# Kernel optimization log

Measured on AMD Instinct MI355X. Metric: run time of the kernel, lower is better.

The kernel has to match this reference:

```python
import jax, jax.numpy as jnp
import numpy as np

NB_FEATURES = 256
DIM_HEADS = 64
KERNEL_EPS = 1e-4


def _gaussian_orthogonal_random_matrix(nb_rows, nb_cols, seed=0):
    # Mirrors gaussian_orthogonal_random_matrix with scaling=0, qr_uniform_q=False.
    rng = np.random.default_rng(seed)
    blocks = []
    for _ in range(nb_rows // nb_cols):
        a = rng.standard_normal((nb_cols, nb_cols))
        qm, _ = np.linalg.qr(a)
        blocks.append(qm.T)
    rem = nb_rows - (nb_rows // nb_cols) * nb_cols
    if rem > 0:
        a = rng.standard_normal((nb_cols, nb_cols))
        qm, _ = np.linalg.qr(a)
        blocks.append(qm.T[:rem])
    final = np.concatenate(blocks, axis=0)
    multiplier = np.linalg.norm(rng.standard_normal((nb_rows, nb_cols)), axis=1)
    return (multiplier[:, None] * final).astype(np.float32)


def setup_inputs() -> dict:
    key = jax.random.key(0)
    kq, kk, kv = jax.random.split(key, 3)
    shape = (2, 16, 4096, DIM_HEADS)  # [b, h, n, dim_heads]
    q = jax.random.normal(kq, shape, dtype=jnp.float32)
    k = jax.random.normal(kk, shape, dtype=jnp.float32)
    v = jax.random.normal(kv, shape, dtype=jnp.float32)
    projection = jnp.asarray(_gaussian_orthogonal_random_matrix(NB_FEATURES, DIM_HEADS))
    return {"q": q, "k": k, "v": v, "projection": projection}


def _softmax_kernel(x, projection, is_query):
    # x: [b,h,n,d]; projection: [j,d]
    d = x.shape[-1]
    data_normalizer = d ** -0.25
    ratio = projection.shape[0] ** -0.5
    data_dash = jnp.einsum('bhnd,jd->bhnj', data_normalizer * x, projection)
    diag = jnp.sum(x * x, axis=-1, keepdims=True) * (0.5 * data_normalizer ** 2)  # [b,h,n,1]
    if is_query:
        m = jnp.max(data_dash, axis=-1, keepdims=True)
    else:
        m = jnp.max(data_dash)
    return ratio * (jnp.exp(data_dash - diag - m) + KERNEL_EPS)


def reference(q, k, v, projection):
    qp = _softmax_kernel(q, projection, is_query=True)   # [b,h,n,j]
    kp = _softmax_kernel(k, projection, is_query=False)  # [b,h,n,j]
    k_sum = jnp.sum(kp, axis=-2)                          # [b,h,j]
    d_inv = 1.0 / jnp.einsum('bhnj,bhj->bhn', qp, k_sum)  # [b,h,n]
    context = jnp.einsum('bhnj,bhne->bhje', kp, v)        # [b,h,j,e]
    out = jnp.einsum('bhje,bhnj,bhn->bhne', context, qp, d_inv)
    return out
```

## Files before the change

### kernel.cpp

```cpp
#include <hip/hip_runtime.h>

#define NFEAT 256
#define DHEAD 64
#define NSEQ  4096
#define NHEADS 32

constexpr float NORM_C  = 0.35355339059327373f;
constexpr float RATIO_C = 0.0625f;
constexpr float DIAG_C  = 0.0625f;
constexpr float KEPS_C  = 1e-4f;

using v8s = __attribute__((ext_vector_type(8))) short;
using v4f = __attribute__((ext_vector_type(4))) float;
union Frag8 { v8s v; ushort u[8]; };

__device__ __forceinline__ ushort bf16h(float x) {
  unsigned u = __float_as_uint(x);
  return (ushort)((u + 0x7FFFu + ((u >> 16) & 1)) >> 16);
}
__device__ __forceinline__ float bf16f(ushort h) {
  return __uint_as_float(((unsigned)h) << 16);
}
__device__ __forceinline__ unsigned enc_f(float f) {
  unsigned u = __float_as_uint(f);
  return (u & 0x80000000u) ? ~u : (u | 0x80000000u);
}
__device__ __forceinline__ float dec_f(unsigned e) {
  return (e & 0x80000000u) ? __uint_as_float(e ^ 0x80000000u) : __uint_as_float(~e);
}

#define MFMA(a, b, c) __builtin_amdgcn_mfma_f32_16x16x32_bf16((a), (b), (c), 0, 0, 0)

__global__ void prep_kernel(const float* __restrict__ proj,
                            ushort* __restrict__ P2hi, ushort* __restrict__ P2lo) {
  int i = blockIdx.x * 256 + threadIdx.x;
  if (i < NFEAT * DHEAD) {
    int j = i >> 6, d = i & 63;
    float x = NORM_C * proj[i];
    ushort h = bf16h(x);
    int off = ((d >> 3) * NFEAT + j) * 8 + (d & 7);
    P2hi[off] = h;
    P2lo[off] = bf16h(x - bf16f(h));
  }
}

__global__ __launch_bounds__(256, 2) void kmax_kernel(
    const float* __restrict__ kk, const ushort* __restrict__ P2hi,
    const ushort* __restrict__ P2lo, unsigned* __restrict__ kmax_u) {
  __shared__ __align__(16) ushort PhiL[NFEAT * DHEAD];
  __shared__ __align__(16) ushort PloL[NFEAT * DHEAD];
  __shared__ float wred[4];
  const int t = threadIdx.x, lane = t & 63, w = t >> 6;
  const int cl = lane & 15, q = lane >> 4;
  const int mw = w & 1, jw = w >> 1;
  const int head = blockIdx.x >> 4, slab = blockIdx.x & 15;
  for (int i = t; i < 4096; i += 256) {
    ((float4*)PhiL)[i] = ((const float4*)P2hi)[i];
    ((float4*)PloL)[i] = ((const float4*)P2lo)[i];
  }
  const float* abase =
      kk + ((size_t)(head * NSEQ + slab * 256 + mw * 16 + cl)) * DHEAD + q * 8;
  float4 pa0 = *(const float4*)(abase);
  float4 pa1 = *(const float4*)(abase + 4);
  float4 pa2 = *(const float4*)(abase + 32);
  float4 pa3 = *(const float4*)(abase + 36);
  __syncthreads();
  float mx = -3.0e38f;
  for (int c = 0; c < 8; ++c) {
    float af[2][8] = {{pa0.x, pa0.y, pa0.z, pa0.w, pa1.x, pa1.y, pa1.z, pa1.w},
                      {pa2.x, pa2.y, pa2.z, pa2.w, pa3.x, pa3.y, pa3.z, pa3.w}};
    Frag8 ah[2], al[2];
#pragma unroll
    for (int ks = 0; ks < 2; ++ks)
#pragma unroll
      for (int i = 0; i < 8; ++i) {
        ushort h = bf16h(af[ks][i]);
        ah[ks].u[i] = h;
        al[ks].u[i] = bf16h(af[ks][i] - bf16f(h));
      }
    if (c < 7) {
      const float* nx = abase + (size_t)(c + 1) * 32 * DHEAD;
      pa0 = *(const float4*)(nx);
      pa1 = *(const float4*)(nx + 4);
      pa2 = *(const float4*)(nx + 32);
      pa3 = *(const float4*)(nx + 36);
    }
    v4f acc[8];
#pragma unroll
    for (int jt = 0; jt < 8; ++jt) acc[jt] = (v4f){0.f, 0.f, 0.f, 0.f};
#pragma unroll
    for (int ks = 0; ks < 2; ++ks)
#pragma unroll
      for (int jt = 0; jt < 8; ++jt) {
        int pidx = ((ks * 4 + q) * NFEAT + jw * 128 + jt * 16 + cl) * 8;
        v8s bh = *(const v8s*)&PhiL[pidx];
        v8s bl = *(const v8s*)&PloL[pidx];
        acc[jt] = MFMA(ah[ks].v, bh, acc[jt]);
        acc[jt] = MFMA(ah[ks].v, bl, acc[jt]);
        acc[jt] = MFMA(al[ks].v, bh, acc[jt]);
      }
#pragma unroll
    for (int jt = 0; jt < 8; ++jt)
#pragma unroll
      for (int r = 0; r < 4; ++r) mx = fmaxf(mx, acc[jt][r]);
  }
  for (int s = 1; s < 64; s <<= 1) mx = fmaxf(mx, __shfl_xor(mx, s));
  if (lane == 0) wred[w] = mx;
  __syncthreads();
  if (t == 0)
    atomicMax(kmax_u,
              enc_f(fmaxf(fmaxf(wred[0], wred[1]), fmaxf(wred[2], wred[3]))));
}

#define KPS 40
#define VTS 40
__global__ __launch_bounds__(512, 2) void kctx_kernel(
    const float* __restrict__ kk, const float* __restrict__ vv,
    const ushort* __restrict__ P2hi, const ushort* __restrict__ P2lo,
    const unsigned* __restrict__ kmax_u, float* __restrict__ ksum,
    float* __restrict__ ctx) {
  __shared__ __align__(16) ushort PhiL[NFEAT * DHEAD];
  __shared__ __align__(16) ushort PloL[NFEAT * DHEAD];
  __shared__ __align__(16) ushort kphi[NFEAT * KPS];
  __shared__ __align__(16) ushort kplo[NFEAT * KPS];
  __shared__ __align__(16) ushort vthi[DHEAD * VTS];
  __shared__ __align__(16) ushort vtlo[DHEAD * VTS];
  __shared__ float diag[32];
  const int t = threadIdx.x, lane = t & 63, w = t >> 6;
  const int cl = lane & 15, q = lane >> 4;
  const int mw = w & 1, jq = w >> 1;
  const int head = blockIdx.x >> 3, slab = blockIdx.x & 7;
  const float m = dec_f(*kmax_u);
  for (int i = t; i < 4096; i += 512) {
    ((float4*)PhiL)[i] = ((const float4*)P2hi)[i];
    ((float4*)PloL)[i] = ((const float4*)P2lo)[i];
  }
  float ksacc[4] = {0.f, 0.f, 0.f, 0.f};
  v4f ctxacc[4][2];
#pragma unroll
  for (int jj = 0; jj < 4; ++jj)
#pragma unroll
    for (int et = 0; et < 2; ++et) ctxacc[jj][et] = (v4f){0.f, 0.f, 0.f, 0.f};

  const float* abase =
      kk + ((size_t)(head * NSEQ + slab * 512 + mw * 16 + cl)) * DHEAD + q * 8;
  const int vrow = t >> 4, ve0 = (t & 15) * 4;
  const float* vbase =
      vv + ((size_t)(head * NSEQ + slab * 512 + vrow)) * DHEAD + ve0;
  float4 pa0 = *(const float4*)(abase);
  float4 pa1 = *(const float4*)(abase + 4);
  float4 pa2 = *(const float4*)(abase + 32);
  float4 pa3 = *(const float4*)(abase + 36);
  float4 pv0 = *(const float4*)(vbase);

  for (int c = 0; c < 16; ++c) {
    __syncthreads();
    {
      float fv[4] = {pv0.x, pv0.y, pv0.z, pv0.w};
#pragma unroll
      for (int cc = 0; cc < 4; ++cc) {
        int e = ve0 + cc;
        ushort h = bf16h(fv[cc]);
        vthi[e * VTS + vrow] = h;
        vtlo[e * VTS + vrow] = bf16h(fv[cc] - bf16f(h));
      }
    }
    float af[2][8] = {{pa0.x, pa0.y, pa0.z, pa0.w, pa1.x, pa1.y, pa1.z, pa1.w},
                      {pa2.x, pa2.y, pa2.z, pa2.w, pa3.x, pa3.y, pa3.z, pa3.w}};
    Frag8 ah[2], al[2];
    float ssq = 0.f;
#pragma unroll
    for (int ks = 0; ks < 2; ++ks)
#pragma unroll
      for (int i = 0; i < 8; ++i) {
        float x = af[ks][i];
        ssq = fmaf(x, x, ssq);
        ushort h = bf16h(x);
        ah[ks].u[i] = h;
        al[ks].u[i] = bf16h(x - bf16f(h));
      }
    if (c < 15) {
      const float* nx = abase + (size_t)(c + 1) * 32 * DHEAD;
      pa0 = *(const float4*)(nx);
      pa1 = *(const float4*)(nx + 4);
      pa2 = *(const float4*)(nx + 32);
      pa3 = *(const float4*)(nx + 36);
      pv0 = *(const float4*)(vbase + (size_t)(c + 1) * 32 * DHEAD);
    }
    v4f acc[4];
#pragma unroll
    for (int jt = 0; jt < 4; ++jt) acc[jt] = (v4f){0.f, 0.f, 0.f, 0.f};
#pragma unroll
    for (int ks = 0; ks < 2; ++ks)
#pragma unroll
      for (int jt = 0; jt < 4; ++jt) {
        int pidx = ((ks * 4 + q) * NFEAT + jq * 64 + jt * 16 + cl) * 8;
        v8s bh = *(const v8s*)&PhiL[pidx];
        v8s bl = *(const v8s*)&PloL[pidx];
        acc[jt] = MFMA(ah[ks].v, bh, acc[jt]);
        acc[jt] = MFMA(ah[ks].v, bl, acc[jt]);
        acc[jt] = MFMA(al[ks].v, bh, acc[jt]);
      }
    {
      float s2 = ssq;
      s2 += __shfl_xor(s2, 16);
      s2 += __shfl_xor(s2, 32);
      if (jq == 0 && q == 0) diag[mw * 16 + cl] = DIAG_C * s2;
    }
    __syncthreads();
#pragma unroll
    for (int jt = 0; jt < 4; ++jt) {
      int j = jq * 64 + jt * 16 + cl;
      float kv[4];
#pragma unroll
      for (int r = 0; r < 4; ++r) {
        int row = mw * 16 + q * 4 + r;
        float e_ = RATIO_C * (__expf(acc[jt][r] - diag[row] - m) + KEPS_C);
        kv[r] = e_;
        ksacc[jt] += e_;
      }
#pragma unroll
      for (int p = 0; p < 2; ++p) {
        ushort h0 = bf16h(kv[2 * p]), h1 = bf16h(kv[2 * p + 1]);
        ushort l0 = bf16h(kv[2 * p] - bf16f(h0));
        ushort l1 = bf16h(kv[2 * p + 1] - bf16f(h1));
        int ui = j * KPS + mw * 16 + q * 4 + 2 * p;
        *(uint*)&kphi[ui] = (uint)h0 | ((uint)h1 << 16);
        *(uint*)&kplo[ui] = (uint)l0 | ((uint)l1 << 16);
      }
    }
    __syncthreads();
    const int eh = w & 1, jq3 = w >> 1;
    v8s bhv[2], blv[2];
#pragma unroll
    for (int et = 0; et < 2; ++et) {
      int e = (eh * 2 + et) * 16 + cl;
      bhv[et] = *(const v8s*)&vthi[e * VTS + q * 8];
      blv[et] = *(const v8s*)&vtlo[e * VTS + q * 8];
    }
#pragma unroll
    for (int jj = 0; jj < 4; ++jj) {
      int jrow = jq3 * 64 + jj * 16 + cl;
      v8s ah2 = *(const v8s*)&kphi[jrow * KPS + q * 8];
      v8s al2 = *(const v8s*)&kplo[jrow * KPS + q * 8];
#pragma unroll
      for (int et = 0; et < 2; ++et) {
        ctxacc[jj][et] = MFMA(ah2, bhv[et], ctxacc[jj][et]);
        ctxacc[jj][et] = MFMA(ah2, blv[et], ctxacc[jj][et]);
        ctxacc[jj][et] = MFMA(al2, bhv[et], ctxacc[jj][et]);
      }
    }
  }
#pragma unroll
  for (int jt = 0; jt < 4; ++jt) {
    float s = ksacc[jt];
    s += __shfl_xor(s, 16);
    s += __shfl_xor(s, 32);
    if (q == 0) atomicAdd(&ksum[head * NFEAT + jq * 64 + jt * 16 + cl], s);
  }
  {
    const int eh = w & 1, jq3 = w >> 1;
#pragma unroll
    for (int jj = 0; jj < 4; ++jj)
#pragma unroll
      for (int et = 0; et < 2; ++et)
#pragma unroll
        for (int r = 0; r < 4; ++r) {
          int j = jq3 * 64 + jj * 16 + q * 4 + r;
          int e = (eh * 2 + et) * 16 + cl;
          atomicAdd(&ctx[((size_t)head * NFEAT + j) * DHEAD + e],
                    ctxacc[jj][et][r]);
        }
  }
}

__global__ void ctxprep_kernel(const float* __restrict__ ctx,
                               ushort* __restrict__ ctxThi,
                               ushort* __restrict__ ctxTlo) {
  __shared__ float tile[64 * 65];
  const int head = blockIdx.x >> 2, jb = blockIdx.x & 3, t = threadIdx.x;
#pragma unroll
  for (int i = 0; i < 16; ++i) {
    int idx = t + i * 256;
    int jj = idx >> 6, e = idx & 63;
    tile[jj * 65 + e] = ctx[((size_t)head * NFEAT + jb * 64 + jj) * DHEAD + e];
  }
  __syncthreads();
#pragma unroll
  for (int i = 0; i < 16; ++i) {
    int idx = t + i * 256;
    int e = idx >> 6, jj = idx & 63;
    float x = tile[jj * 65 + e];
    ushort h = bf16h(x);
    size_t o = ((size_t)head * DHEAD + e) * NFEAT + jb * 64 + jj;
    ctxThi[o] = h;
    ctxTlo[o] = bf16h(x - bf16f(h));
  }
}

#define QPS 264
#define OS 68
__global__ __launch_bounds__(512, 2) void qout_kernel(
    const float* __restrict__ qq, const ushort* __restrict__ P2hi,
    const ushort* __restrict__ P2lo, const float* __restrict__ ksum,
    const ushort* __restrict__ ctxThi, const ushort* __restrict__ ctxTlo,
    float* __restrict__ out) {
  __shared__ __align__(16) ushort PhiL[NFEAT * DHEAD];
  __shared__ __align__(16) ushort PloL[NFEAT * DHEAD];
  __shared__ __align__(16) ushort qphi[32 * QPS];
  __shared__ __align__(16) ushort qplo[32 * QPS];
  __shared__ __align__(16) float souts[32 * OS];
  __shared__ float diag[32];
  __shared__ float mpart[4][32], dpart[4][32];
  const int t = threadIdx.x, lane = t & 63, w = t >> 6;
  const int cl = lane & 15, q = lane >> 4;
  const int mw = w & 1, jq = w >> 1;
  const int mw3 = w & 1, et3 = w >> 1;
  const int head = blockIdx.x >> 3, slab = blockIdx.x & 7;
  for (int i = t; i < 4096; i += 512) {
    ((float4*)PhiL)[i] = ((const float4*)P2hi)[i];
    ((float4*)PloL)[i] = ((const float4*)P2lo)[i];
  }
  float ksl[4];
#pragma unroll
  for (int jt = 0; jt < 4; ++jt)
    ksl[jt] = ksum[head * NFEAT + jq * 64 + jt * 16 + cl];
  v8s bhr[8], blr[8];
  {
    const size_t bo = ((size_t)head * DHEAD + et3 * 16 + cl) * NFEAT + q * 8;
#pragma unroll
    for (int ks8 = 0; ks8 < 8; ++ks8) {
      bhr[ks8] = *(const v8s*)(ctxThi + bo + ks8 * 32);
      blr[ks8] = *(const v8s*)(ctxTlo + bo + ks8 * 32);
    }
  }
  const float* abase =
      qq + ((size_t)(head * NSEQ + slab * 512 + mw * 16 + cl)) * DHEAD + q * 8;
  float4 pa0 = *(const float4*)(abase);
  float4 pa1 = *(const float4*)(abase + 4);
  float4 pa2 = *(const float4*)(abase + 32);
  float4 pa3 = *(const float4*)(abase + 36);
  __syncthreads();

  for (int c = 0; c < 16; ++c) {
    const int row0 = slab * 512 + c * 32;
    float af[2][8] = {{pa0.x, pa0.y, pa0.z, pa0.w, pa1.x, pa1.y, pa1.z, pa1.w},
                      {pa2.x, pa2.y, pa2.z, pa2.w, pa3.x, pa3.y, pa3.z, pa3.w}};
    Frag8 ah[2], al[2];
    float ssq = 0.f;
#pragma unroll
    for (int ks = 0; ks < 2; ++ks)
#pragma unroll
      for (int i = 0; i < 8; ++i) {
        float x = af[ks][i];
        ssq = fmaf(x, x, ssq);
        ushort h = bf16h(x);
        ah[ks].u[i] = h;
        al[ks].u[i] = bf16h(x - bf16f(h));
      }
    if (c < 15) {
      const float* nx = abase + (size_t)(c + 1) * 32 * DHEAD;
      pa0 = *(const float4*)(nx);
      pa1 = *(const float4*)(nx + 4);
      pa2 = *(const float4*)(nx + 32);
      pa3 = *(const float4*)(nx + 36);
    }
    v4f acc[4];
#pragma unroll
    for (int jt = 0; jt < 4; ++jt) acc[jt] = (v4f){0.f, 0.f, 0.f, 0.f};
#pragma unroll
    for (int ks = 0; ks < 2; ++ks)
#pragma unroll
      for (int jt = 0; jt < 4; ++jt) {
        int pidx = ((ks * 4 + q) * NFEAT + jq * 64 + jt * 16 + cl) * 8;
        v8s bh = *(const v8s*)&PhiL[pidx];
        v8s bl = *(const v8s*)&PloL[pidx];
        acc[jt] = MFMA(ah[ks].v, bh, acc[jt]);
        acc[jt] = MFMA(ah[ks].v, bl, acc[jt]);
        acc[jt] = MFMA(al[ks].v, bh, acc[jt]);
      }
    {
      float s2 = ssq;
      s2 += __shfl_xor(s2, 16);
      s2 += __shfl_xor(s2, 32);
      if (jq == 0 && q == 0) diag[mw * 16 + cl] = DIAG_C * s2;
    }
#pragma unroll
    for (int r = 0; r < 4; ++r) {
      float mr = acc[0][r];
#pragma unroll
      for (int jt = 1; jt < 4; ++jt) mr = fmaxf(mr, acc[jt][r]);
      mr = fmaxf(mr, __shfl_xor(mr, 1));
      mr = fmaxf(mr, __shfl_xor(mr, 2));
      mr = fmaxf(mr, __shfl_xor(mr, 4));
      mr = fmaxf(mr, __shfl_xor(mr, 8));
      if (cl == 0) mpart[jq][mw * 16 + q * 4 + r] = mr;
    }
    __syncthreads();
#pragma unroll
    for (int r = 0; r < 4; ++r) {
      int row = mw * 16 + q * 4 + r;
      float mm = fmaxf(fmaxf(mpart[0][row], mpart[1][row]),
                       fmaxf(mpart[2][row], mpart[3][row])) + diag[row];
      float ds = 0.f;
#pragma unroll
      for (int jt = 0; jt < 4; ++jt) {
        float qv = RATIO_C * (__expf(acc[jt][r] - mm) + KEPS_C);
        ds = fmaf(qv, ksl[jt], ds);
        int j = jq * 64 + jt * 16 + cl;
        ushort h = bf16h(qv);
        qphi[row * QPS + j] = h;
        qplo[row * QPS + j] = bf16h(qv - bf16f(h));
      }
      ds += __shfl_xor(ds, 1);
      ds += __shfl_xor(ds, 2);
      ds += __shfl_xor(ds, 4);
      ds += __shfl_xor(ds, 8);
      if (cl == 0) dpart[jq][row] = ds;
    }
    __syncthreads();
    v4f oacc = (v4f){0.f, 0.f, 0.f, 0.f};
#pragma unroll
    for (int ks8 = 0; ks8 < 8; ++ks8) {
      v8s ahq = *(const v8s*)&qphi[(mw3 * 16 + cl) * QPS + ks8 * 32 + q * 8];
      v8s alq = *(const v8s*)&qplo[(mw3 * 16 + cl) * QPS + ks8 * 32 + q * 8];
      oacc = MFMA(ahq, bhr[ks8], oacc);
      oacc = MFMA(ahq, blr[ks8], oacc);
      oacc = MFMA(alq, bhr[ks8], oacc);
    }
#pragma unroll
    for (int r = 0; r < 4; ++r) {
      int row = mw3 * 16 + q * 4 + r;
      float di = 1.0f / (dpart[0][row] + dpart[1][row] + dpart[2][row] +
                         dpart[3][row]);
      souts[row * OS + et3 * 16 + cl] = oacc[r] * di;
    }
    __syncthreads();
    {
      const int row = t >> 4, eo = (t & 15) * 4;
      float4 rr = *(const float4*)&souts[row * OS + eo];
      *(float4*)(out + ((size_t)(head * NSEQ + row0 + row)) * DHEAD + eo) = rr;
    }
    __syncthreads();
  }
}

extern "C" void kernel_launch(void* const* d_in, const int* in_sizes, int n_in,
                              void* d_out, int out_size, void* d_ws, size_t ws_size,
                              hipStream_t stream) {
  (void)in_sizes; (void)n_in; (void)out_size; (void)ws_size;
  const float* q = (const float*)d_in[0];
  const float* k = (const float*)d_in[1];
  const float* v = (const float*)d_in[2];
  const float* proj = (const float*)d_in[3];
  float* out = (float*)d_out;
  unsigned char* ws = (unsigned char*)d_ws;
  unsigned* kmax_u = (unsigned*)ws;
  float* ksum = (float*)(ws + 256);
  float* ctx = (float*)(ws + 33024);
  ushort* P2hi = (ushort*)(ws + 2130176);
  ushort* P2lo = (ushort*)(ws + 2162944);
  ushort* ctxThi = (ushort*)(ws + 2195712);
  ushort* ctxTlo = (ushort*)(ws + 3244288);
  hipMemsetAsync(d_ws, 0, 2130176, stream);
  hipLaunchKernelGGL(prep_kernel, dim3(64), dim3(256), 0, stream, proj, P2hi, P2lo);
  hipLaunchKernelGGL(kmax_kernel, dim3(512), dim3(256), 0, stream, k, P2hi, P2lo,
                     kmax_u);
  hipLaunchKernelGGL(kctx_kernel, dim3(256), dim3(512), 0, stream, k, v, P2hi,
                     P2lo, kmax_u, ksum, ctx);
  hipLaunchKernelGGL(ctxprep_kernel, dim3(128), dim3(256), 0, stream, ctx,
                     ctxThi, ctxTlo);
  hipLaunchKernelGGL(qout_kernel, dim3(256), dim3(512), 0, stream, q, P2hi,
                     P2lo, ksum, ctxThi, ctxTlo, out);
}
```

Before: 262.4 us.

## Read projection fragments from global/L2 instead of LDS, double grid, raise occupancy

Removes the 64 KB per-block LDS staging of the hi/lo projection matrices in all three main kernels and loads the MFMA B fragments straight from global memory, relying on cache. Freeing the LDS allows launch bounds of 4 blocks per CU, and the kctx and qout grids are doubled to 512 blocks with half the sequence slab each. kmax now uses 512 threads with 4-wide feature tiles. qout reloads the ctx fragments every iteration instead of keeping them in registers, and splits the output accumulation into two independent MFMA chains. The trade-off is more global/L2 traffic for the projection and ctx fragments in exchange for higher occupancy and no LDS preload or barrier.

Measured after the change: 357.0 us. +36.1%, slower.

```diff
diff --git a/kernel.cpp b/kernel.cpp
--- a/kernel.cpp
+++ b/kernel.cpp
@@ -3,7 +3,6 @@
 #define NFEAT 256
 #define DHEAD 64
 #define NSEQ  4096
-#define NHEADS 32
 
 constexpr float NORM_C  = 0.35355339059327373f;
 constexpr float RATIO_C = 0.0625f;
@@ -44,29 +43,27 @@
   }
 }
 
-__global__ __launch_bounds__(256, 2) void kmax_kernel(
+__global__ __launch_bounds__(512, 4) void kmax_kernel(
     const float* __restrict__ kk, const ushort* __restrict__ P2hi,
     const ushort* __restrict__ P2lo, unsigned* __restrict__ kmax_u) {
-  __shared__ __align__(16) ushort PhiL[NFEAT * DHEAD];
-  __shared__ __align__(16) ushort PloL[NFEAT * DHEAD];
-  __shared__ float wred[4];
+  __shared__ float wred[8];
   const int t = threadIdx.x, lane = t & 63, w = t >> 6;
   const int cl = lane & 15, q = lane >> 4;
-  const int mw = w & 1, jw = w >> 1;
+  const int mw = w & 1, jq = w >> 1;
   const int head = blockIdx.x >> 4, slab = blockIdx.x & 15;
-  for (int i = t; i < 4096; i += 256) {
-    ((float4*)PhiL)[i] = ((const float4*)P2hi)[i];
-    ((float4*)PloL)[i] = ((const float4*)P2lo)[i];
-  }
+  const ushort* ph0 = P2hi + (size_t)(q * NFEAT + jq * 64 + cl) * 8;
+  const ushort* ph1 = ph0 + (size_t)4 * NFEAT * 8;
+  const ushort* pl0 = P2lo + (size_t)(q * NFEAT + jq * 64 + cl) * 8;
+  const ushort* pl1 = pl0 + (size_t)4 * NFEAT * 8;
   const float* abase =
       kk + ((size_t)(head * NSEQ + slab * 256 + mw * 16 + cl)) * DHEAD + q * 8;
   float4 pa0 = *(const float4*)(abase);
   float4 pa1 = *(const float4*)(abase + 4);
   float4 pa2 = *(const float4*)(abase + 32);
   float4 pa3 = *(const float4*)(abase + 36);
-  __syncthreads();
   float mx = -3.0e38f;
   for (int c = 0; c < 8; ++c) {
+    asm volatile("" : "+v"(ph0), "+v"(ph1), "+v"(pl0), "+v"(pl1));
     float af[2][8] = {{pa0.x, pa0.y, pa0.z, pa0.w, pa1.x, pa1.y, pa1.z, pa1.w},
                       {pa2.x, pa2.y, pa2.z, pa2.w, pa3.x, pa3.y, pa3.z, pa3.w}};
     Frag8 ah[2], al[2];
@@ -85,42 +82,45 @@
       pa2 = *(const float4*)(nx + 32);
       pa3 = *(const float4*)(nx + 36);
     }
-    v4f acc[8];
-#pragma unroll
-    for (int jt = 0; jt < 8; ++jt) acc[jt] = (v4f){0.f, 0.f, 0.f, 0.f};
-#pragma unroll
-    for (int ks = 0; ks < 2; ++ks)
-#pragma unroll
-      for (int jt = 0; jt < 8; ++jt) {
-        int pidx = ((ks * 4 + q) * NFEAT + jw * 128 + jt * 16 + cl) * 8;
-        v8s bh = *(const v8s*)&PhiL[pidx];
-        v8s bl = *(const v8s*)&PloL[pidx];
+    v4f acc[4];
+#pragma unroll
+    for (int jt = 0; jt < 4; ++jt) acc[jt] = (v4f){0.f, 0.f, 0.f, 0.f};
+#pragma unroll
+    for (int ks = 0; ks < 2; ++ks) {
+      const ushort* bhp = ks ? ph1 : ph0;
+      const ushort* blp = ks ? pl1 : pl0;
+#pragma unroll
+      for (int jt = 0; jt < 4; ++jt) {
+        v8s bh = *(const v8s*)(bhp + jt * 128);
+        v8s bl = *(const v8s*)(blp + jt * 128);
         acc[jt] = MFMA(ah[ks].v, bh, acc[jt]);
         acc[jt] = MFMA(ah[ks].v, bl, acc[jt]);
         acc[jt] = MFMA(al[ks].v, bh, acc[jt]);
       }
-#pragma unroll
-    for (int jt = 0; jt < 8; ++jt)
+    }
+#pragma unroll
+    for (int jt = 0; jt < 4; ++jt)
 #pragma unroll
       for (int r = 0; r < 4; ++r) mx = fmaxf(mx, acc[jt][r]);
   }
   for (int s = 1; s < 64; s <<= 1) mx = fmaxf(mx, __shfl_xor(mx, s));
   if (lane == 0) wred[w] = mx;
   __syncthreads();
-  if (t == 0)
-    atomicMax(kmax_u,
-              enc_f(fmaxf(fmaxf(wred[0], wred[1]), fmaxf(wred[2], wred[3]))));
+  if (t == 0) {
+    float r = wred[0];
+#pragma unroll
+    for (int i = 1; i < 8; ++i) r = fmaxf(r, wred[i]);
+    atomicMax(kmax_u, enc_f(r));
+  }
 }
 
 #define KPS 40
 #define VTS 40
-__global__ __launch_bounds__(512, 2) void kctx_kernel(
+__global__ __launch_bounds__(512, 4) void kctx_kernel(
     const float* __restrict__ kk, const float* __restrict__ vv,
     const ushort* __restrict__ P2hi, const ushort* __restrict__ P2lo,
     const unsigned* __restrict__ kmax_u, float* __restrict__ ksum,
     float* __restrict__ ctx) {
-  __shared__ __align__(16) ushort PhiL[NFEAT * DHEAD];
-  __shared__ __align__(16) ushort PloL[NFEAT * DHEAD];
   __shared__ __align__(16) ushort kphi[NFEAT * KPS];
   __shared__ __align__(16) ushort kplo[NFEAT * KPS];
   __shared__ __align__(16) ushort vthi[DHEAD * VTS];
@@ -129,12 +129,12 @@
   const int t = threadIdx.x, lane = t & 63, w = t >> 6;
   const int cl = lane & 15, q = lane >> 4;
   const int mw = w & 1, jq = w >> 1;
-  const int head = blockIdx.x >> 3, slab = blockIdx.x & 7;
+  const int head = blockIdx.x >> 4, slab = blockIdx.x & 15;
   const float m = dec_f(*kmax_u);
-  for (int i = t; i < 4096; i += 512) {
-    ((float4*)PhiL)[i] = ((const float4*)P2hi)[i];
-    ((float4*)PloL)[i] = ((const float4*)P2lo)[i];
-  }
+  const ushort* ph0 = P2hi + (size_t)(q * NFEAT + jq * 64 + cl) * 8;
+  const ushort* ph1 = ph0 + (size_t)4 * NFEAT * 8;
+  const ushort* pl0 = P2lo + (size_t)(q * NFEAT + jq * 64 + cl) * 8;
+  const ushort* pl1 = pl0 + (size_t)4 * NFEAT * 8;
   float ksacc[4] = {0.f, 0.f, 0.f, 0.f};
   v4f ctxacc[4][2];
 #pragma unroll
@@ -143,18 +143,19 @@
     for (int et = 0; et < 2; ++et) ctxacc[jj][et] = (v4f){0.f, 0.f, 0.f, 0.f};
 
   const float* abase =
-      kk + ((size_t)(head * NSEQ + slab * 512 + mw * 16 + cl)) * DHEAD + q * 8;
+      kk + ((size_t)(head * NSEQ + slab * 256 + mw * 16 + cl)) * DHEAD + q * 8;
   const int vrow = t >> 4, ve0 = (t & 15) * 4;
   const float* vbase =
-      vv + ((size_t)(head * NSEQ + slab * 512 + vrow)) * DHEAD + ve0;
+      vv + ((size_t)(head * NSEQ + slab * 256 + vrow)) * DHEAD + ve0;
   float4 pa0 = *(const float4*)(abase);
   float4 pa1 = *(const float4*)(abase + 4);
   float4 pa2 = *(const float4*)(abase + 32);
   float4 pa3 = *(const float4*)(abase + 36);
   float4 pv0 = *(const float4*)(vbase);
 
-  for (int c = 0; c < 16; ++c) {
-    __syncthreads();
+  for (int c = 0; c < 8; ++c) {
+    __syncthreads();
+    asm volatile("" : "+v"(ph0), "+v"(ph1), "+v"(pl0), "+v"(pl1));
     {
       float fv[4] = {pv0.x, pv0.y, pv0.z, pv0.w};
 #pragma unroll
@@ -179,7 +180,7 @@
         ah[ks].u[i] = h;
         al[ks].u[i] = bf16h(x - bf16f(h));
       }
-    if (c < 15) {
+    if (c < 7) {
       const float* nx = abase + (size_t)(c + 1) * 32 * DHEAD;
       pa0 = *(const float4*)(nx);
       pa1 = *(const float4*)(nx + 4);
@@ -191,16 +192,18 @@
 #pragma unroll
     for (int jt = 0; jt < 4; ++jt) acc[jt] = (v4f){0.f, 0.f, 0.f, 0.f};
 #pragma unroll
-    for (int ks = 0; ks < 2; ++ks)
+    for (int ks = 0; ks < 2; ++ks) {
+      const ushort* bhp = ks ? ph1 : ph0;
+      const ushort* blp = ks ? pl1 : pl0;
 #pragma unroll
       for (int jt = 0; jt < 4; ++jt) {
-        int pidx = ((ks * 4 + q) * NFEAT + jq * 64 + jt * 16 + cl) * 8;
-        v8s bh = *(const v8s*)&PhiL[pidx];
-        v8s bl = *(const v8s*)&PloL[pidx];
+        v8s bh = *(const v8s*)(bhp + jt * 128);
+        v8s bl = *(const v8s*)(blp + jt * 128);
         acc[jt] = MFMA(ah[ks].v, bh, acc[jt]);
         acc[jt] = MFMA(ah[ks].v, bl, acc[jt]);
         acc[jt] = MFMA(al[ks].v, bh, acc[jt]);
       }
+    }
     {
       float s2 = ssq;
       s2 += __shfl_xor(s2, 16);
@@ -300,13 +303,11 @@
 
 #define QPS 264
 #define OS 68
-__global__ __launch_bounds__(512, 2) void qout_kernel(
+__global__ __launch_bounds__(512, 4) void qout_kernel(
     const float* __restrict__ qq, const ushort* __restrict__ P2hi,
     const ushort* __restrict__ P2lo, const float* __restrict__ ksum,
     const ushort* __restrict__ ctxThi, const ushort* __restrict__ ctxTlo,
     float* __restrict__ out) {
-  __shared__ __align__(16) ushort PhiL[NFEAT * DHEAD];
-  __shared__ __align__(16) ushort PloL[NFEAT * DHEAD];
   __shared__ __align__(16) ushort qphi[32 * QPS];
   __shared__ __align__(16) ushort qplo[32 * QPS];
   __shared__ __align__(16) float souts[32 * OS];
@@ -316,34 +317,30 @@
   const int cl = lane & 15, q = lane >> 4;
   const int mw = w & 1, jq = w >> 1;
   const int mw3 = w & 1, et3 = w >> 1;
-  const int head = blockIdx.x >> 3, slab = blockIdx.x & 7;
-  for (int i = t; i < 4096; i += 512) {
-    ((float4*)PhiL)[i] = ((const float4*)P2hi)[i];
-    ((float4*)PloL)[i] = ((const float4*)P2lo)[i];
-  }
+  const int head = blockIdx.x >> 4, slab = blockIdx.x & 15;
+  const ushort* ph0 = P2hi + (size_t)(q * NFEAT + jq * 64 + cl) * 8;
+  const ushort* ph1 = ph0 + (size_t)4 * NFEAT * 8;
+  const ushort* pl0 = P2lo + (size_t)(q * NFEAT + jq * 64 + cl) * 8;
+  const ushort* pl1 = pl0 + (size_t)4 * NFEAT * 8;
+  const ushort* cbh =
+      ctxThi + ((size_t)head * DHEAD + et3 * 16 + cl) * NFEAT + q * 8;
+  const ushort* cbl =
+      ctxTlo + ((size_t)head * DHEAD + et3 * 16 + cl) * NFEAT + q * 8;
   float ksl[4];
 #pragma unroll
   for (int jt = 0; jt < 4; ++jt)
     ksl[jt] = ksum[head * NFEAT + jq * 64 + jt * 16 + cl];
-  v8s bhr[8], blr[8];
-  {
-    const size_t bo = ((size_t)head * DHEAD + et3 * 16 + cl) * NFEAT + q * 8;
-#pragma unroll
-    for (int ks8 = 0; ks8 < 8; ++ks8) {
-      bhr[ks8] = *(const v8s*)(ctxThi + bo + ks8 * 32);
-      blr[ks8] = *(const v8s*)(ctxTlo + bo + ks8 * 32);
-    }
-  }
   const float* abase =
-      qq + ((size_t)(head * NSEQ + slab * 512 + mw * 16 + cl)) * DHEAD + q * 8;
+      qq + ((size_t)(head * NSEQ + slab * 256 + mw * 16 + cl)) * DHEAD + q * 8;
   float4 pa0 = *(const float4*)(abase);
   float4 pa1 = *(const float4*)(abase + 4);
   float4 pa2 = *(const float4*)(abase + 32);
   float4 pa3 = *(const float4*)(abase + 36);
-  __syncthreads();
-
-  for (int c = 0; c < 16; ++c) {
-    const int row0 = slab * 512 + c * 32;
+
+  for (int c = 0; c < 8; ++c) {
+    const int row0 = slab * 256 + c * 32;
+    asm volatile("" : "+v"(ph0), "+v"(ph1), "+v"(pl0), "+v"(pl1),
+                      "+v"(cbh), "+v"(cbl));
     float af[2][8] = {{pa0.x, pa0.y, pa0.z, pa0.w, pa1.x, pa1.y, pa1.z, pa1.w},
                       {pa2.x, pa2.y, pa2.z, pa2.w, pa3.x, pa3.y, pa3.z, pa3.w}};
     Frag8 ah[2], al[2];
@@ -358,7 +355,7 @@
         ah[ks].u[i] = h;
         al[ks].u[i] = bf16h(x - bf16f(h));
       }
-    if (c < 15) {
+    if (c < 7) {
       const float* nx = abase + (size_t)(c + 1) * 32 * DHEAD;
       pa0 = *(const float4*)(nx);
       pa1 = *(const float4*)(nx + 4);
@@ -369,16 +366,18 @@
 #pragma unroll
     for (int jt = 0; jt < 4; ++jt) acc[jt] = (v4f){0.f, 0.f, 0.f, 0.f};
 #pragma unroll
-    for (int ks = 0; ks < 2; ++ks)
+    for (int ks = 0; ks < 2; ++ks) {
+      const ushort* bhp = ks ? ph1 : ph0;
+      const ushort* blp = ks ? pl1 : pl0;
 #pragma unroll
       for (int jt = 0; jt < 4; ++jt) {
-        int pidx = ((ks * 4 + q) * NFEAT + jq * 64 + jt * 16 + cl) * 8;
-        v8s bh = *(const v8s*)&PhiL[pidx];
-        v8s bl = *(const v8s*)&PloL[pidx];
+        v8s bh = *(const v8s*)(bhp + jt * 128);
+        v8s bl = *(const v8s*)(blp + jt * 128);
         acc[jt] = MFMA(ah[ks].v, bh, acc[jt]);
         acc[jt] = MFMA(ah[ks].v, bl, acc[jt]);
         acc[jt] = MFMA(al[ks].v, bh, acc[jt]);
       }
+    }
     {
       float s2 = ssq;
       s2 += __shfl_xor(s2, 16);
@@ -397,6 +396,12 @@
       if (cl == 0) mpart[jq][mw * 16 + q * 4 + r] = mr;
     }
     __syncthreads();
+    v8s bhr[8], blr[8];
+#pragma unroll
+    for (int ks8 = 0; ks8 < 8; ++ks8) {
+      bhr[ks8] = *(const v8s*)(cbh + ks8 * 32);
+      blr[ks8] = *(const v8s*)(cbl + ks8 * 32);
+    }
 #pragma unroll
     for (int r = 0; r < 4; ++r) {
       int row = mw * 16 + q * 4 + r;
@@ -419,21 +424,29 @@
       if (cl == 0) dpart[jq][row] = ds;
     }
     __syncthreads();
-    v4f oacc = (v4f){0.f, 0.f, 0.f, 0.f};
-#pragma unroll
-    for (int ks8 = 0; ks8 < 8; ++ks8) {
-      v8s ahq = *(const v8s*)&qphi[(mw3 * 16 + cl) * QPS + ks8 * 32 + q * 8];
-      v8s alq = *(const v8s*)&qplo[(mw3 * 16 + cl) * QPS + ks8 * 32 + q * 8];
-      oacc = MFMA(ahq, bhr[ks8], oacc);
-      oacc = MFMA(ahq, blr[ks8], oacc);
-      oacc = MFMA(alq, bhr[ks8], oacc);
+    v4f oaccA = (v4f){0.f, 0.f, 0.f, 0.f};
+    v4f oaccB = (v4f){0.f, 0.f, 0.f, 0.f};
+#pragma unroll
+    for (int ks8 = 0; ks8 < 8; ks8 += 2) {
+      v8s ahq0 = *(const v8s*)&qphi[(mw3 * 16 + cl) * QPS + ks8 * 32 + q * 8];
+      v8s alq0 = *(const v8s*)&qplo[(mw3 * 16 + cl) * QPS + ks8 * 32 + q * 8];
+      v8s ahq1 =
+          *(const v8s*)&qphi[(mw3 * 16 + cl) * QPS + (ks8 + 1) * 32 + q * 8];
+      v8s alq1 =
+          *(const v8s*)&qplo[(mw3 * 16 + cl) * QPS + (ks8 + 1) * 32 + q * 8];
+      oaccA = MFMA(ahq0, bhr[ks8], oaccA);
+      oaccA = MFMA(ahq0, blr[ks8], oaccA);
+      oaccA = MFMA(alq0, bhr[ks8], oaccA);
+      oaccB = MFMA(ahq1, bhr[ks8 + 1], oaccB);
+      oaccB = MFMA(ahq1, blr[ks8 + 1], oaccB);
+      oaccB = MFMA(alq1, bhr[ks8 + 1], oaccB);
     }
 #pragma unroll
     for (int r = 0; r < 4; ++r) {
       int row = mw3 * 16 + q * 4 + r;
       float di = 1.0f / (dpart[0][row] + dpart[1][row] + dpart[2][row] +
                          dpart[3][row]);
-      souts[row * OS + et3 * 16 + cl] = oacc[r] * di;
+      souts[row * OS + et3 * 16 + cl] = (oaccA[r] + oaccB[r]) * di;
     }
     __syncthreads();
     {
@@ -464,12 +477,12 @@
   ushort* ctxTlo = (ushort*)(ws + 3244288);
   hipMemsetAsync(d_ws, 0, 2130176, stream);
   hipLaunchKernelGGL(prep_kernel, dim3(64), dim3(256), 0, stream, proj, P2hi, P2lo);
-  hipLaunchKernelGGL(kmax_kernel, dim3(512), dim3(256), 0, stream, k, P2hi, P2lo,
+  hipLaunchKernelGGL(kmax_kernel, dim3(512), dim3(512), 0, stream, k, P2hi, P2lo,
                      kmax_u);
-  hipLaunchKernelGGL(kctx_kernel, dim3(256), dim3(512), 0, stream, k, v, P2hi,
+  hipLaunchKernelGGL(kctx_kernel, dim3(512), dim3(512), 0, stream, k, v, P2hi,
                      P2lo, kmax_u, ksum, ctx);
   hipLaunchKernelGGL(ctxprep_kernel, dim3(128), dim3(256), 0, stream, ctx,
                      ctxThi, ctxTlo);
-  hipLaunchKernelGGL(qout_kernel, dim3(256), dim3(512), 0, stream, q, P2hi,
+  hipLaunchKernelGGL(qout_kernel, dim3(512), dim3(512), 0, stream, q, P2hi,
                      P2lo, ksum, ctxThi, ctxTlo, out);
 }
```
